# Optimization experiments

Hardware: AMD Instinct MI355X
Metric: run time of the kernel (lower is better)

## Reference

```python
import jax, jax.numpy as jnp
import numpy as np

D = 128
H = 8
B = 4
L = 2048


def setup_inputs() -> dict:
    key = jax.random.key(0)
    ks = jax.random.split(key, 5)
    s = 1.0 / np.sqrt(D)
    x = jax.random.normal(ks[0], (B, L, D), dtype=jnp.float32)
    Wq = jax.random.normal(ks[1], (D, D * H), dtype=jnp.float32) * s
    Wk = jax.random.normal(ks[2], (D, D * H), dtype=jnp.float32) * s
    Wv = jax.random.normal(ks[3], (D, D * H), dtype=jnp.float32) * s
    Wu = jax.random.normal(ks[4], (D * H, D), dtype=jnp.float32) * (1.0 / np.sqrt(D * H))
    bu = jnp.zeros((D,), dtype=jnp.float32)
    return {"x": x, "Wq": Wq, "Wk": Wk, "Wv": Wv, "Wu": Wu, "bu": bu}


def reference(x, Wq, Wk, Wv, Wu, bu):
    b, l, d = x.shape
    h = H
    # project and split heads: [b, l, h, d] -> [b, h, l, d]
    q = (x @ Wq).reshape(b, l, h, d).transpose(0, 2, 1, 3)
    k = (x @ Wk).reshape(b, l, h, d).transpose(0, 2, 1, 3)
    v = (x @ Wv).reshape(b, l, h, d).transpose(0, 2, 1, 3)
    scores = jnp.einsum("bhqd,bhkd->bhqk", q, k) / jnp.sqrt(jnp.float32(d))
    w = jax.nn.softmax(scores, axis=-1)
    out = jnp.einsum("bhqk,bhkd->bhqd", w, v)  # [b, h, l, d]
    out = out.transpose(0, 2, 1, 3).reshape(b, l, h * d)
    return out @ Wu + bu
```

## Files before the change

kernel.cpp:

```cpp
#include <hip/hip_runtime.h>
#include <stdint.h>

#define D_ 128
#define H_ 8
#define B_ 4
#define L_ 2048
#define NH (B_*H_)

typedef __bf16 bf16x8 __attribute__((ext_vector_type(8)));
typedef float f32x4 __attribute__((ext_vector_type(4)));
typedef float f32x16 __attribute__((ext_vector_type(16)));
typedef unsigned short u16;
typedef u16 u16x2 __attribute__((ext_vector_type(2)));
typedef u16 u16x4 __attribute__((ext_vector_type(4)));
typedef u16 u16x8 __attribute__((ext_vector_type(8)));
typedef uint32_t u32x2 __attribute__((ext_vector_type(2)));
typedef uint32_t u32x4 __attribute__((ext_vector_type(4)));
typedef float fvec4 __attribute__((ext_vector_type(4)));

__device__ __forceinline__ u16 f2b(float f){
    uint32_t u = __builtin_bit_cast(uint32_t, f);
    u += 0x7fffu + ((u >> 16) & 1u);
    return (u16)(u >> 16);
}
__device__ __forceinline__ u16 f2b_native(float f){
    return __builtin_bit_cast(u16, (__bf16)f);
}
__device__ __forceinline__ uint32_t pk2(float a, float b){
    u16x2 v = { f2b_native(a), f2b_native(b) };
    return __builtin_bit_cast(uint32_t, v);
}
__device__ __forceinline__ float ex2(float x){
#if __has_builtin(__builtin_amdgcn_exp2f)
    return __builtin_amdgcn_exp2f(x);
#else
    return exp2f(x);
#endif
}
__device__ __forceinline__ u32x2 permswap(uint32_t a, uint32_t b){
#if __has_builtin(__builtin_amdgcn_permlane32_swap)
    return __builtin_amdgcn_permlane32_swap(a, b, false, false);
#else
    asm volatile("v_permlane32_swap_b32 %0, %1" : "+v"(a), "+v"(b));
    u32x2 r; r[0] = a; r[1] = b; return r;
#endif
}
__device__ __forceinline__ bf16x8 asbf(u16x8 v){ return __builtin_bit_cast(bf16x8, v); }
#define MFMA(a,b,c)   __builtin_amdgcn_mfma_f32_16x16x32_bf16((a),(b),(c),0,0,0)
#define MFMA32(a,b,c) __builtin_amdgcn_mfma_f32_32x32x16_bf16((a),(b),(c),0,0,0)

__device__ __forceinline__ void gld16(const u16* g, u16* l){
    __builtin_amdgcn_global_load_lds(
        (const __attribute__((address_space(1))) void*)g,
        (__attribute__((address_space(3))) void*)l, 16, 0, 0);
}

__global__ __launch_bounds__(256)
void cvt_all(const float* __restrict__ x, const float* __restrict__ Wq,
             const float* __restrict__ Wk, const float* __restrict__ Wv,
             const float* __restrict__ Wu,
             u16* __restrict__ xb, u16* __restrict__ wT, u16* __restrict__ wuT)
{
    const int blk = blockIdx.x;
    const int t = threadIdx.x;
    if (blk < 512){
        size_t i = ((size_t)blk*256 + t)*8;
        fvec4 lo = *(const fvec4*)&x[i];
        fvec4 hi = *(const fvec4*)&x[i+4];
        u16x8 u;
        for (int j=0;j<4;++j){ u[j]=f2b(lo[j]); u[4+j]=f2b(hi[j]); }
        *(u16x8*)&xb[i] = u;
        return;
    }
    __shared__ __align__(16) u16 T[128][144];
    const int b = blk - 512;
    const float* src; int ld, coff, roff; u16* dst;
    if (b < 24){
        int mat = b>>3, head = b&7;
        src = (mat==0)?Wq:((mat==1)?Wk:Wv); ld = D_*H_; coff = head*128; roff = 0;
        dst = wT + (size_t)b*16384;
    } else {
        src = Wu; ld = D_; coff = 0; roff = (b-24)*128;
        dst = wuT + (size_t)(b-24)*16384;
    }
    for (int it=0; it<16; ++it){
        int k = it*8 + (t>>5), n0 = (t&31)*4;
        fvec4 wv = *(const fvec4*)&src[(size_t)(roff+k)*ld + coff + n0];
        for (int i=0;i<4;++i) T[n0+i][k] = f2b(wv[i]);
    }
    __syncthreads();
    for (int it=0; it<8; ++it){
        int gi = it*256 + t; int n = gi>>4, g = gi&15;
        *(u16x8*)&dst[n*128 + g*8] = *(const u16x8*)&T[n][(g^(n&7))*8];
    }
}

__global__ __launch_bounds__(256)
void qkv_proj(const u16* __restrict__ xb, const u16* __restrict__ wT,
              u16* __restrict__ q_ws, u16* __restrict__ k_ws, u16* __restrict__ v_ws)
{
    const int head = blockIdx.x;
    const int rt   = blockIdx.y;
    const int mat  = blockIdx.z;

    __shared__ __align__(16) u16 Xs[128*128];
    __shared__ __align__(16) u16 Ws[128*128];

    const int t = threadIdx.x;
    const int row0 = rt*128;
    const u16* wsrc = wT + (size_t)(mat*8 + head)*16384;

    for (int it=0; it<8; ++it){
        int gi = it*256 + t;
        int r = gi>>4, g = gi&15;
        gld16(&xb[(size_t)(row0+r)*D_ + ((g ^ (r&7))*8)], &Xs[(it*256 + (t>>6)*64)*8]);
        gld16(&wsrc[gi*8],                                &Ws[(it*256 + (t>>6)*64)*8]);
    }
    asm volatile("s_waitcnt vmcnt(0)" ::: "memory");
    __builtin_amdgcn_s_barrier();

    const int wave = t>>6, lane = t&63;
    const int wr = wave>>1, wc = wave&1;
    const int lrow = lane&15, lgrp = lane>>4;
    const int swz = lrow&7;

    f32x4 acc[4][4] = {};
    #pragma unroll
    for (int kc=0;kc<4;++kc){
        const int gd = kc*4 + lgrp;
        bf16x8 a[4], bfr[4];
        #pragma unroll
        for (int mr=0;mr<4;++mr)
            a[mr] = asbf(*(const u16x8*)&Xs[(wr*64+mr*16+lrow)*128 + ((gd ^ swz)*8)]);
        #pragma unroll
        for (int nr=0;nr<4;++nr)
            bfr[nr] = asbf(*(const u16x8*)&Ws[(wc*64+nr*16+lrow)*128 + ((gd ^ swz)*8)]);
        #pragma unroll
        for (int mr=0;mr<4;++mr)
            #pragma unroll
            for (int nr=0;nr<4;++nr)
                acc[mr][nr] = MFMA(a[mr], bfr[nr], acc[mr][nr]);
    }

    const float qscale = 0.12751879455370425f;
    for (int mr=0;mr<4;++mr){
        for (int nr=0;nr<4;++nr){
            f32x4 v = acc[mr][nr];
            int baserow = row0 + wr*64 + mr*16 + lgrp*4;
            int cd = wc*64 + nr*16 + lrow;
            int b  = baserow / L_;
            int l  = baserow % L_;
            int bh = b*H_ + head;
            if (mat==2){
                u16x4 pv;
                for (int r=0;r<4;++r) pv[r] = f2b(v[r]);
                *(u16x4*)&v_ws[((size_t)bh*D_ + cd)*L_ + l] = pv;
            } else {
                u16* dst = (mat==0) ? q_ws : k_ws;
                for (int r=0;r<4;++r){
                    float f = v[r];
                    if (mat==0) f *= qscale;
                    dst[((size_t)bh*L_ + (l + r))*D_ + cd] = f2b(f);
                }
            }
        }
    }
}

__global__ __launch_bounds__(512)
void attn(const u16* __restrict__ q_ws, const u16* __restrict__ k_ws,
          const u16* __restrict__ v_ws, u16* __restrict__ o_ws)
{
    const int wg = ((blockIdx.x & 7) << 5) | (blockIdx.x >> 3);
    const int qt = wg & 7;
    const int bh = wg >> 3;

    const int t = threadIdx.x, wave = t>>6, lane = t&63;
    const int q31 = lane & 31;
    const int hi  = lane >> 5;
    const int swq = q31 & 7;

    __shared__ __align__(16) u16 Kb[3][64*128];
    __shared__ __align__(16) u16 Vb[3][128*64];

    const int q0 = qt*256 + wave*32;

    bf16x8 qf[8];
    #pragma unroll
    for (int ks=0; ks<8; ++ks)
        qf[ks] = asbf(*(const u16x8*)&q_ws[((size_t)bh*L_ + q0 + q31)*D_ + ks*16 + hi*8]);

    const u16* kp = k_ws + (size_t)bh*L_*D_;
    const u16* vp = v_ws + (size_t)bh*D_*L_;
    int koff[2], voff[2];
    #pragma unroll
    for (int i=0;i<2;++i){
        int f = i*512 + t;
        int kr = f>>4, kc = f&15;
        koff[i] = kr*128 + ((kc ^ (kr&7))*8);
        int vr = f>>3, vc = f&7;
        voff[i] = vr*L_ + ((vc ^ (vr&7))*8);
    }

    auto stage = [&](int buf){
        #pragma unroll
        for (int i=0;i<2;++i){
            gld16(kp + koff[i], &Kb[buf][(i*512 + wave*64)*8]);
            gld16(vp + voff[i], &Vb[buf][(i*512 + wave*64)*8]);
        }
        kp += 64*D_;
        vp += 64;
    };

    float lsA = 0.f, lsB = 0.f;
    f32x16 o4[4] = {};

    stage(0);
    stage(1);
    asm volatile("s_waitcnt vmcnt(4)" ::: "memory");
    __builtin_amdgcn_s_barrier();

    for (int kt=0; kt<L_/64; ++kt){
        const int cur = kt % 3;
        if (kt < L_/64 - 2) stage((kt+2) % 3);

        f32x16 s0a = {}, s0b = {}, s1a = {}, s1b = {};
        __builtin_amdgcn_s_setprio(1);
        #pragma unroll
        for (int ks=0; ks<4; ++ks){
            bf16x8 ka0 = asbf(*(const u16x8*)&Kb[cur][q31*128      + (((ks*2+hi)     ^ swq)*8)]);
            bf16x8 ka1 = asbf(*(const u16x8*)&Kb[cur][q31*128      + ((((ks+4)*2+hi) ^ swq)*8)]);
            bf16x8 kb0 = asbf(*(const u16x8*)&Kb[cur][(32+q31)*128 + (((ks*2+hi)     ^ swq)*8)]);
            bf16x8 kb1 = asbf(*(const u16x8*)&Kb[cur][(32+q31)*128 + ((((ks+4)*2+hi) ^ swq)*8)]);
            s0a = MFMA32(ka0, qf[ks],   s0a);
            s0b = MFMA32(ka1, qf[ks+4], s0b);
            s1a = MFMA32(kb0, qf[ks],   s1a);
            s1b = MFMA32(kb1, qf[ks+4], s1b);
        }
        __builtin_amdgcn_s_setprio(0);
        f32x16 s0 = s0a + s0b;
        f32x16 s1 = s1a + s1b;

        #define SM_PV(SREG, KS) do { \
            float p0 = ex2(SREG[((KS&1)*8)+0]); \
            float p1 = ex2(SREG[((KS&1)*8)+1]); \
            float p2 = ex2(SREG[((KS&1)*8)+2]); \
            float p3 = ex2(SREG[((KS&1)*8)+3]); \
            float p4 = ex2(SREG[((KS&1)*8)+4]); \
            float p5 = ex2(SREG[((KS&1)*8)+5]); \
            float p6 = ex2(SREG[((KS&1)*8)+6]); \
            float p7 = ex2(SREG[((KS&1)*8)+7]); \
            lsA += (p0+p1)+(p2+p3); \
            lsB += (p4+p5)+(p6+p7); \
            uint32_t cA = pk2(p0,p1), cB = pk2(p2,p3); \
            uint32_t cC = pk2(p4,p5), cD = pk2(p6,p7); \
            u32x2 r0 = permswap(cA, cC); \
            u32x2 r1 = permswap(cB, cD); \
            u32x4 wv; \
            wv[0] = r0[0];  wv[1] = r1[0]; \
            wv[2] = r0[1];  wv[3] = r1[1]; \
            bf16x8 pa = __builtin_bit_cast(bf16x8, wv); \
            __builtin_amdgcn_s_setprio(1); \
            _Pragma("unroll") \
            for (int nc2=0; nc2<4; ++nc2){ \
                bf16x8 vb = asbf(*(const u16x8*)&Vb[cur][ (nc2*32+q31)*64 + (((KS*2+hi) ^ swq)*8) ]); \
                o4[nc2] = MFMA32(pa, vb, o4[nc2]); \
            } \
            __builtin_amdgcn_s_setprio(0); \
        } while(0)

        SM_PV(s0, 0);
        SM_PV(s0, 1);
        SM_PV(s1, 2);
        SM_PV(s1, 3);
        #undef SM_PV

        if (kt < L_/64 - 1){
            if (kt < L_/64 - 2) asm volatile("s_waitcnt vmcnt(4)" ::: "memory");
            else                asm volatile("s_waitcnt vmcnt(0)" ::: "memory");
            __builtin_amdgcn_s_barrier();
        }
    }

    float lsum = lsA + lsB;
    lsum += __shfl_xor(lsum, 32, 64);
    float inv = 1.0f / lsum;

    const int b = bh / H_, h = bh % H_;
    #pragma unroll
    for (int m=0; m<4; ++m){
        #pragma unroll
        for (int i=0; i<4; ++i){
            const int reg = m*4 + i;
            const int row = i + 8*m + 4*hi;
            float riv = __shfl(inv, row, 64);
            const int l = q0 + row;
            size_t base = ((size_t)(b*L_ + l))*(D_*H_) + h*128 + q31;
            #pragma unroll
            for (int nc2=0; nc2<4; ++nc2)
                o_ws[base + nc2*32] = f2b_native(o4[nc2][reg] * riv);
        }
    }
}

__global__ __launch_bounds__(256)
void out_proj(const u16* __restrict__ o_ws, const u16* __restrict__ wuT,
              const float* __restrict__ bu, float* __restrict__ out)
{
    const int rt = blockIdx.x;
    const int t = threadIdx.x, wave = t>>6, lane = t&63;
    const int wr = wave>>1, wc = wave&1;
    const int lrow = lane&15, lgrp = lane>>4;
    const int swz = lrow&7;

    __shared__ __align__(16) u16 As[2][32*128];
    __shared__ __align__(16) u16 Ws[2][128*128];

    const int row0 = rt*32;
    f32x4 acc[4] = {};

    auto stage = [&](int ks){
        const int buf = ks & 1;
        int gi = t;
        int r = gi>>4, g = gi&15;
        gld16(&o_ws[(size_t)(row0+r)*(D_*H_) + ks*128 + ((g ^ (r&7))*8)], &As[buf][((t>>6)*64)*8]);
        gi = 256 + t;
        r = gi>>4; g = gi&15;
        gld16(&o_ws[(size_t)(row0+r)*(D_*H_) + ks*128 + ((g ^ (r&7))*8)], &As[buf][(256 + (t>>6)*64)*8]);
        const u16* wsrc = wuT + (size_t)ks*16384;
        #pragma unroll
        for (int it=0; it<8; ++it)
            gld16(&wsrc[(it*256 + t)*8], &Ws[buf][(it*256 + (t>>6)*64)*8]);
    };

    stage(0);
    for (int ks=0; ks<8; ++ks){
        const int buf = ks & 1;
        if (ks < 7){
            stage(ks+1);
            asm volatile("s_waitcnt vmcnt(10)" ::: "memory");
        } else {
            asm volatile("s_waitcnt vmcnt(0)" ::: "memory");
        }
        __builtin_amdgcn_s_barrier();

        #pragma unroll
        for (int kc=0;kc<4;++kc){
            const int gd = kc*4 + lgrp;
            bf16x8 a = asbf(*(const u16x8*)&As[buf][(wr*16+lrow)*128 + ((gd ^ swz)*8)]);
            #pragma unroll
            for (int nc=0;nc<4;++nc){
                bf16x8 b = asbf(*(const u16x8*)&Ws[buf][(wc*64+nc*16+lrow)*128 + ((gd ^ swz)*8)]);
                acc[nc] = MFMA(a, b, acc[nc]);
            }
        }
        __builtin_amdgcn_s_barrier();
    }

    for (int nc=0;nc<4;++nc){
        for (int r=0;r<4;++r){
            int row = row0 + wr*16 + lgrp*4 + r;
            int n = wc*64 + nc*16 + lrow;
            out[(size_t)row*D_ + n] = acc[nc][r] + bu[n];
        }
    }
}

extern "C" void kernel_launch(void* const* d_in, const int* in_sizes, int n_in,
                              void* d_out, int out_size, void* d_ws, size_t ws_size,
                              hipStream_t stream)
{
    const float* x  = (const float*)d_in[0];
    const float* Wq = (const float*)d_in[1];
    const float* Wk = (const float*)d_in[2];
    const float* Wv = (const float*)d_in[3];
    const float* Wu = (const float*)d_in[4];
    const float* bu = (const float*)d_in[5];
    float* out = (float*)d_out;

    u16* ws = (u16*)d_ws;
    const size_t SZ = (size_t)NH * L_ * D_;
    u16* q_ws = ws;
    u16* k_ws = q_ws + SZ;
    u16* v_ws = k_ws + SZ;
    u16* o_ws = v_ws + SZ;
    u16* x_bf = o_ws + SZ;
    u16* wT   = x_bf + (size_t)B_*L_*D_;
    u16* wuT  = wT + 24*16384;

    cvt_all<<<dim3(544), 256, 0, stream>>>(x, Wq, Wk, Wv, Wu, x_bf, wT, wuT);
    qkv_proj<<<dim3(H_, (B_*L_)/128, 3), 256, 0, stream>>>(x_bf, wT, q_ws, k_ws, v_ws);
    attn<<<dim3((L_/256)*NH), 512, 0, stream>>>(q_ws, k_ws, v_ws, o_ws);
    out_proj<<<dim3((B_*L_)/32), 256, 0, stream>>>(o_ws, wuT, bu, out);
}
```

Before: 119.9 us.

## Software-pipeline QK^T one tile ahead and deepen K/V staging to four buffers

The attention loop now computes the QK^T scores for the next key tile while doing exp and PV for the current tile. The aim is to let MFMA score work overlap the transcendental and packing work of softmax. The K/V LDS ring grows from three to four buffers, so loads are issued three tiles ahead and the waits are adjusted to match. The cost is more LDS (128KB), more live accumulator registers, and a risk of spills or of the compiler reordering away the intended overlap.

```diff
diff --git a/kernel.cpp b/kernel.cpp
--- a/kernel.cpp
+++ b/kernel.cpp
@@ -180,8 +180,8 @@
     const int hi  = lane >> 5;
     const int swq = q31 & 7;
 
-    __shared__ __align__(16) u16 Kb[3][64*128];
-    __shared__ __align__(16) u16 Vb[3][128*64];
+    __shared__ __align__(16) u16 Kb[4][64*128];
+    __shared__ __align__(16) u16 Vb[4][128*64];
 
     const int q0 = qt*256 + wave*32;
 
@@ -212,34 +212,43 @@
         vp += 64;
     };
 
-    float lsA = 0.f, lsB = 0.f;
-    f32x16 o4[4] = {};
-
-    stage(0);
-    stage(1);
-    asm volatile("s_waitcnt vmcnt(4)" ::: "memory");
-    __builtin_amdgcn_s_barrier();
-
-    for (int kt=0; kt<L_/64; ++kt){
-        const int cur = kt % 3;
-        if (kt < L_/64 - 2) stage((kt+2) % 3);
-
+    auto qkt = [&](int buf, f32x16& S0, f32x16& S1){
         f32x16 s0a = {}, s0b = {}, s1a = {}, s1b = {};
-        __builtin_amdgcn_s_setprio(1);
         #pragma unroll
         for (int ks=0; ks<4; ++ks){
-            bf16x8 ka0 = asbf(*(const u16x8*)&Kb[cur][q31*128      + (((ks*2+hi)     ^ swq)*8)]);
-            bf16x8 ka1 = asbf(*(const u16x8*)&Kb[cur][q31*128      + ((((ks+4)*2+hi) ^ swq)*8)]);
-            bf16x8 kb0 = asbf(*(const u16x8*)&Kb[cur][(32+q31)*128 + (((ks*2+hi)     ^ swq)*8)]);
-            bf16x8 kb1 = asbf(*(const u16x8*)&Kb[cur][(32+q31)*128 + ((((ks+4)*2+hi) ^ swq)*8)]);
+            bf16x8 ka0 = asbf(*(const u16x8*)&Kb[buf][q31*128      + (((ks*2+hi)     ^ swq)*8)]);
+            bf16x8 ka1 = asbf(*(const u16x8*)&Kb[buf][q31*128      + ((((ks+4)*2+hi) ^ swq)*8)]);
+            bf16x8 kb0 = asbf(*(const u16x8*)&Kb[buf][(32+q31)*128 + (((ks*2+hi)     ^ swq)*8)]);
+            bf16x8 kb1 = asbf(*(const u16x8*)&Kb[buf][(32+q31)*128 + ((((ks+4)*2+hi) ^ swq)*8)]);
             s0a = MFMA32(ka0, qf[ks],   s0a);
             s0b = MFMA32(ka1, qf[ks+4], s0b);
             s1a = MFMA32(kb0, qf[ks],   s1a);
             s1b = MFMA32(kb1, qf[ks+4], s1b);
         }
+        S0 = s0a + s0b;
+        S1 = s1a + s1b;
+    };
+
+    float lsA = 0.f, lsB = 0.f;
+    f32x16 o4[4] = {};
+
+    stage(0);
+    stage(1);
+    stage(2);
+    asm volatile("s_waitcnt vmcnt(4)" ::: "memory");
+    __builtin_amdgcn_s_barrier();
+
+    f32x16 sP0, sP1, sN0, sN1;
+    qkt(0, sP0, sP1);
+
+    const int NT = L_/64;
+    for (int kt=0; kt<NT; ++kt){
+        const int cur = kt & 3;
+        if (kt < NT-3) stage((kt+3) & 3);
+
+        __builtin_amdgcn_s_setprio(1);
+        if (kt < NT-1) qkt((kt+1) & 3, sN0, sN1);
         __builtin_amdgcn_s_setprio(0);
-        f32x16 s0 = s0a + s0b;
-        f32x16 s1 = s1a + s1b;
 
         #define SM_PV(SREG, KS) do { \
             float p0 = ex2(SREG[((KS&1)*8)+0]); \
@@ -269,17 +278,19 @@
             __builtin_amdgcn_s_setprio(0); \
         } while(0)
 
-        SM_PV(s0, 0);
-        SM_PV(s0, 1);
-        SM_PV(s1, 2);
-        SM_PV(s1, 3);
+        SM_PV(sP0, 0);
+        SM_PV(sP0, 1);
+        SM_PV(sP1, 2);
+        SM_PV(sP1, 3);
         #undef SM_PV
 
-        if (kt < L_/64 - 1){
-            if (kt < L_/64 - 2) asm volatile("s_waitcnt vmcnt(4)" ::: "memory");
-            else                asm volatile("s_waitcnt vmcnt(0)" ::: "memory");
+        if (kt < NT-1){
+            if (kt <= NT-4) asm volatile("s_waitcnt vmcnt(4)" ::: "memory");
+            else            asm volatile("s_waitcnt vmcnt(0)" ::: "memory");
             __builtin_amdgcn_s_barrier();
         }
+        sP0 = sN0;
+        sP1 = sN1;
     }
 
     float lsum = lsA + lsB;
```

After: 119.3 us. About the same (-0.5%).
